# Optimization experiments

Hardware: AMD Instinct MI355X
Metric: run time of the kernel (lower is better)

## Reference

```python
import jax, jax.numpy as jnp
import numpy as np

EPS = 1e-06

def rotate_half(x):
    d = x.shape[-1] // 2
    return jnp.concatenate([-x[..., d:], x[..., :d]], axis=-1)

def rmsnorm(x, w):
    rms = jnp.sqrt(jnp.mean(x * x, axis=-1, keepdims=True) + EPS)
    return (x / rms) * w

def setup_inputs() -> dict:
    key = jax.random.key(0)
    ks = jax.random.split(key, 12)
    H, Hq, Hkv, Dh, S, C = 2048, 16, 8, 128, 1, 16384
    sc = 0.02
    return {
        "hidden_states": jax.random.normal(ks[0], (1, 1, S, H), jnp.float32),
        "cos": jax.random.uniform(ks[1], (1, 1, S, Dh), jnp.float32),
        "sin": jax.random.uniform(ks[2], (1, 1, S, Dh), jnp.float32),
        "attention_mask": jnp.zeros((1, 1, S, C + S), jnp.float32),
        "k_cache": jax.random.normal(ks[3], (Hkv, Dh, C), jnp.float32),
        "v_cache": jax.random.normal(ks[4], (Hkv, C, Dh), jnp.float32),
        "Wq": jax.random.normal(ks[5], (Hq, Dh, H), jnp.float32) * sc,
        "Wk": jax.random.normal(ks[6], (Hkv, Dh, H), jnp.float32) * sc,
        "Wv": jax.random.normal(ks[7], (Hkv, Dh, H), jnp.float32) * sc,
        "Wo": jax.random.normal(ks[8], (H, Hq * Dh), jnp.float32) * sc,
        "q_norm_w": jnp.ones((Dh,), jnp.float32),
        "k_norm_w": jnp.ones((Dh,), jnp.float32),
    }

def reference(hidden_states, cos, sin, attention_mask, k_cache, v_cache, Wq, Wk, Wv, Wo, q_norm_w, k_norm_w):
    S = hidden_states.shape[2]
    Hq, Dh = Wq.shape[0], Wq.shape[1]
    Hkv = Wk.shape[0]
    g = Hq // Hkv
    x = hidden_states.reshape(S, -1)                      # [S, H]
    # per-head 1x1 conv == per-head linear; batched as einsum
    q = rmsnorm(jnp.einsum('sh,qdh->qsd', x, Wq), q_norm_w)   # [Hq, S, Dh]
    k = rmsnorm(jnp.einsum('sh,kdh->ksd', x, Wk), k_norm_w)   # [Hkv, S, Dh]
    v = jnp.einsum('sh,kdh->ksd', x, Wv)                      # [Hkv, S, Dh]
    c = cos.reshape(S, Dh)
    s = sin.reshape(S, Dh)
    q = q * c + rotate_half(q) * s
    k_new = k * c + rotate_half(k) * s
    # KV cache concat: k stored transposed [Hkv, Dh, C]
    k_full = jnp.concatenate([k_cache, jnp.swapaxes(k_new, 1, 2)], axis=2)  # [Hkv, Dh, C+S]
    v_full = jnp.concatenate([v_cache, v], axis=1)                          # [Hkv, C+S, Dh]
    kf = jnp.repeat(k_full, g, axis=0)                    # GQA expand -> [Hq, Dh, C+S]
    vf = jnp.repeat(v_full, g, axis=0)                    # [Hq, C+S, Dh]
    scaling = Dh ** -0.5
    scores = jnp.einsum('qsd,qdc->qsc', q, kf) * scaling + attention_mask.reshape(1, S, -1)
    probs = jax.nn.softmax(scores, axis=-1)
    out = jnp.einsum('qsc,qcd->qsd', probs, vf)           # [Hq, S, Dh]
    out = jnp.transpose(out, (1, 0, 2)).reshape(S, Hq * Dh)  # head-major last dim
    attn = out @ Wo.T                                     # o_proj 1x1 conv
    return attn.reshape(1, 1, S, -1), k_new, v
```

## Files before the change

### kernel.cpp

```cpp
#include <hip/hip_runtime.h>
#include <math.h>
#include <stddef.h>

#define HQ   16
#define HKV  8
#define DH   128
#define HID  2048
#define CC   16384
#define SPAD 16896
#define NSCH 65
#define NAV  64


__global__ void k_qkv(const float* __restrict__ x,
                      const float* __restrict__ Wq,
                      const float* __restrict__ Wk,
                      const float* __restrict__ Wv,
                      float* __restrict__ raw){
  int wave = threadIdx.x >> 6, lane = threadIdx.x & 63;
  int e = blockIdx.x * 4 + wave;
  const float* W;
  if (e < 2048)      W = Wq + (size_t)e * HID;
  else if (e < 3072) W = Wk + (size_t)(e - 2048) * HID;
  else               W = Wv + (size_t)(e - 3072) * HID;
  float acc = 0.f;
  #pragma unroll
  for (int j = 0; j < 4; ++j){
    int base = (j * 64 + lane) * 8;
    float4 a0 = *(const float4*)(x + base);
    float4 a1 = *(const float4*)(x + base + 4);
    float4 b0 = *(const float4*)(W + base);
    float4 b1 = *(const float4*)(W + base + 4);
    acc += a0.x*b0.x + a0.y*b0.y + a0.z*b0.z + a0.w*b0.w
         + a1.x*b1.x + a1.y*b1.y + a1.z*b1.z + a1.w*b1.w;
  }
  #pragma unroll
  for (int off = 32; off; off >>= 1) acc += __shfl_down(acc, off, 64);
  if (lane == 0) raw[e] = acc;
}

__global__ void k_normrope(const float* __restrict__ raw,
                           const float* __restrict__ cosb,
                           const float* __restrict__ sinb,
                           const float* __restrict__ qw,
                           const float* __restrict__ kw,
                           float* __restrict__ qf,
                           float* __restrict__ kf,
                           float* __restrict__ out){
  __shared__ float lds[DH];
  __shared__ float wsum[2];
  int b = blockIdx.x, t = threadIdx.x;
  if (b >= 24){
    int h = b - 24;
    out[3072 + h * DH + t] = raw[3072 + h * DH + t];
    return;
  }
  bool isq = (b < 16);
  int h = isq ? b : b - 16;
  float val = isq ? raw[h * DH + t] : raw[2048 + h * DH + t];
  float ss = val * val;
  #pragma unroll
  for (int off = 32; off; off >>= 1) ss += __shfl_down(ss, off, 64);
  if ((t & 63) == 0) wsum[t >> 6] = ss;
  __syncthreads();
  float rms = sqrtf((wsum[0] + wsum[1]) / 128.f + 1e-6f);
  float w = isq ? qw[t] : kw[t];
  float normed = val / rms * w;
  lds[t] = normed;
  __syncthreads();
  float rot = (t < 64) ? -lds[t + 64] : lds[t - 64];
  float res = normed * cosb[t] + rot * sinb[t];
  if (isq) qf[h * DH + t] = res;
  else { kf[h * DH + t] = res; out[2048 + h * DH + t] = res; }
}

__global__ void k_scores(const float* __restrict__ qf,
                         const float* __restrict__ kf,
                         const float* __restrict__ kcache,
                         const float* __restrict__ mask,
                         float* __restrict__ S,
                         float* __restrict__ spart){
  __shared__ float q_s[2][DH];
  __shared__ float red[8];
  int kv = blockIdx.x / NSCH, ch = blockIdx.x % NSCH;
  int c0 = ch * 256;
  int t = threadIdx.x;
  q_s[t >> 7][t & 127] = qf[(kv * 2 + (t >> 7)) * DH + (t & 127)];
  __syncthreads();
  const float scale = 0.08838834764831845f;

  int c = c0 + t;
  float s0, s1;
  if (c < CC){
    const float* kp = kcache + (size_t)kv * DH * CC + c;
    float a0 = 0.f, a1 = 0.f;
    #pragma unroll 8
    for (int d = 0; d < DH; ++d){
      float kd = kp[(size_t)d * CC];
      a0 += q_s[0][d] * kd;
      a1 += q_s[1][d] * kd;
    }
    float mk = mask[c];
    s0 = a0 * scale + mk;
    s1 = a1 * scale + mk;
    S[(size_t)(kv * 2)     * SPAD + c] = s0;
    S[(size_t)(kv * 2 + 1) * SPAD + c] = s1;
  } else if (c == CC){
    const float* kp = kf + kv * DH;
    float a0 = 0.f, a1 = 0.f;
    #pragma unroll 8
    for (int d = 0; d < DH; ++d){
      float kd = kp[d];
      a0 += q_s[0][d] * kd;
      a1 += q_s[1][d] * kd;
    }
    float mk = mask[c];
    s0 = a0 * scale + mk;
    s1 = a1 * scale + mk;
    S[(size_t)(kv * 2)     * SPAD + c] = s0;
    S[(size_t)(kv * 2 + 1) * SPAD + c] = s1;
  } else {
    s0 = -1e30f; s1 = -1e30f;
  }

  int wv = t >> 6, ln = t & 63;
  float lmax0 = s0, lmax1 = s1;
  #pragma unroll
  for (int off = 32; off; off >>= 1){
    lmax0 = fmaxf(lmax0, __shfl_down(lmax0, off, 64));
    lmax1 = fmaxf(lmax1, __shfl_down(lmax1, off, 64));
  }
  if (ln == 0){ red[wv] = lmax0; red[4 + wv] = lmax1; }
  __syncthreads();
  float m0 = fmaxf(fmaxf(red[0], red[1]), fmaxf(red[2], red[3]));
  float m1 = fmaxf(fmaxf(red[4], red[5]), fmaxf(red[6], red[7]));
  float ls0 = __expf(s0 - m0);
  float ls1 = __expf(s1 - m1);
  #pragma unroll
  for (int off = 32; off; off >>= 1){
    ls0 += __shfl_down(ls0, off, 64);
    ls1 += __shfl_down(ls1, off, 64);
  }
  __syncthreads();
  if (ln == 0){ red[wv] = ls0; red[4 + wv] = ls1; }
  __syncthreads();
  if (t == 0){
    float l0 = red[0] + red[1] + red[2] + red[3];
    float l1 = red[4] + red[5] + red[6] + red[7];
    spart[((size_t)(kv * 2)     * NSCH + ch) * 2]     = m0;
    spart[((size_t)(kv * 2)     * NSCH + ch) * 2 + 1] = l0;
    spart[((size_t)(kv * 2 + 1) * NSCH + ch) * 2]     = m1;
    spart[((size_t)(kv * 2 + 1) * NSCH + ch) * 2 + 1] = l1;
  }
}

__global__ void k_red(const float* __restrict__ spart, float2* __restrict__ ML){
  int qh = blockIdx.x, lane = threadIdx.x;
  float M = -1e30f, L = 0.f;
  for (int j = lane; j < NSCH; j += 64){
    float mj = spart[((size_t)qh * NSCH + j) * 2];
    float lj = spart[((size_t)qh * NSCH + j) * 2 + 1];
    float nM = fmaxf(M, mj);
    L = L * __expf(M - nM) + lj * __expf(mj - nM);
    M = nM;
  }
  #pragma unroll
  for (int off = 32; off; off >>= 1){
    float Mo = __shfl_down(M, off, 64);
    float Lo = __shfl_down(L, off, 64);
    float nM = fmaxf(M, Mo);
    L = L * __expf(M - nM) + Lo * __expf(Mo - nM);
    M = nM;
  }
  if (lane == 0) ML[qh] = make_float2(M, L);
}

__global__ void k_av(const float* __restrict__ S,
                     const float2* __restrict__ ML,
                     const float* __restrict__ vcache,
                     float* __restrict__ opart){
  __shared__ float part[2][8][DH];
  int kv = blockIdx.x >> 6, ch = blockIdx.x & 63;
  int c0 = ch << 8;
  int t = threadIdx.x;
  int s = t >> 5, d4 = (t & 31) * 4;
  float2 ml0 = ML[kv * 2], ml1 = ML[kv * 2 + 1];
  float M0 = ml0.x, Li0 = 1.f / ml0.y;
  float M1 = ml1.x, Li1 = 1.f / ml1.y;
  const float* S0 = S + (size_t)(kv * 2)     * SPAD;
  const float* S1 = S + (size_t)(kv * 2 + 1) * SPAD;
  const float* vbase = vcache + (size_t)kv * CC * DH + d4;
  float4 a0 = make_float4(0.f, 0.f, 0.f, 0.f);
  float4 a1 = make_float4(0.f, 0.f, 0.f, 0.f);
  #pragma unroll 4
  for (int i = 0; i < 32; ++i){
    int c = c0 + i * 8 + s;
    float p0 = __expf(S0[c] - M0);
    float p1 = __expf(S1[c] - M1);
    float4 v = *(const float4*)(vbase + (size_t)c * DH);
    a0.x += p0 * v.x; a0.y += p0 * v.y; a0.z += p0 * v.z; a0.w += p0 * v.w;
    a1.x += p1 * v.x; a1.y += p1 * v.y; a1.z += p1 * v.z; a1.w += p1 * v.w;
  }
  *(float4*)&part[0][s][d4] = a0;
  *(float4*)&part[1][s][d4] = a1;
  __syncthreads();
  {
    int hh = t >> 7, d = t & 127;
    float o = 0.f;
    #pragma unroll
    for (int ss = 0; ss < 8; ++ss) o += part[hh][ss][d];
    float Li = hh ? Li1 : Li0;
    int qh = kv * 2 + hh;
    opart[((size_t)qh * NAV + ch) * DH + d] = o * Li;
  }
}

__global__ void k_osum(const float* __restrict__ opart,
                       const float* __restrict__ S,
                       const float2* __restrict__ ML,
                       const float* __restrict__ vnew,
                       float* __restrict__ attn_in){
  int qh = blockIdx.x, d = threadIdx.x;
  int kv = qh >> 1;
  float o = 0.f;
  for (int ch = 0; ch < NAV; ++ch)
    o += opart[((size_t)qh * NAV + ch) * DH + d];
  float2 ml = ML[qh];
  float pn = __expf(S[(size_t)qh * SPAD + CC] - ml.x) / ml.y;
  o += pn * vnew[kv * DH + d];
  attn_in[qh * DH + d] = o;
}

__global__ void k_oproj(const float* __restrict__ attn_in,
                        const float* __restrict__ Wo,
                        float* __restrict__ out){
  int wave = threadIdx.x >> 6, lane = threadIdx.x & 63;
  int e = blockIdx.x * 4 + wave;
  const float* W = Wo + (size_t)e * HID;
  float acc = 0.f;
  #pragma unroll
  for (int j = 0; j < 4; ++j){
    int base = (j * 64 + lane) * 8;
    float4 a0 = *(const float4*)(attn_in + base);
    float4 a1 = *(const float4*)(attn_in + base + 4);
    float4 b0 = *(const float4*)(W + base);
    float4 b1 = *(const float4*)(W + base + 4);
    acc += a0.x*b0.x + a0.y*b0.y + a0.z*b0.z + a0.w*b0.w
         + a1.x*b1.x + a1.y*b1.y + a1.z*b1.z + a1.w*b1.w;
  }
  #pragma unroll
  for (int off = 32; off; off >>= 1) acc += __shfl_down(acc, off, 64);
  if (lane == 0) out[e] = acc;
}

extern "C" void kernel_launch(void* const* d_in, const int* in_sizes, int n_in,
                              void* d_out, int out_size, void* d_ws, size_t ws_size,
                              hipStream_t stream){
  const float* x    = (const float*)d_in[0];
  const float* cosb = (const float*)d_in[1];
  const float* sinb = (const float*)d_in[2];
  const float* mask = (const float*)d_in[3];
  const float* kc   = (const float*)d_in[4];
  const float* vc   = (const float*)d_in[5];
  const float* Wq   = (const float*)d_in[6];
  const float* Wk   = (const float*)d_in[7];
  const float* Wv   = (const float*)d_in[8];
  const float* Wo   = (const float*)d_in[9];
  const float* qw   = (const float*)d_in[10];
  const float* kw   = (const float*)d_in[11];
  float* out = (float*)d_out;
  float* ws = (float*)d_ws;
  float* raw     = ws;
  float* qf      = ws + 4096;
  float* kf      = ws + 6144;
  float* S       = ws + 8192;
  float* spart   = ws + 278528;
  float2* ML     = (float2*)(ws + 280608);
  float* opart   = ws + 280640;
  float* attn_in = ws + 411712;

  k_qkv     <<<1024, 256, 0, stream>>>(x, Wq, Wk, Wv, raw);
  k_normrope<<<32,   128, 0, stream>>>(raw, cosb, sinb, qw, kw, qf, kf, out);
  k_scores  <<<HKV * NSCH, 256, 0, stream>>>(qf, kf, kc, mask, S, spart);
  k_red     <<<HQ, 64, 0, stream>>>(spart, ML);
  k_av      <<<HKV * NAV, 256, 0, stream>>>(S, ML, vc, opart);
  k_osum    <<<HQ, DH, 0, stream>>>(opart, S, ML, raw + 3072, attn_in);
  k_oproj   <<<512, 256, 0, stream>>>(attn_in, Wo, out);
}
```

Measured before the change: 217.8 us.

## Fuse scores, softmax and AV into one split-KV flash-decode kernel

Replaces the separate score, max/sum reduction, AV and output-sum kernels with one flash-decoding kernel. Each block computes scores for a 256-key chunk using float4 K loads split across four d-groups, keeps the probabilities in shared memory, and immediately accumulates P·V. A combine kernel then merges the per-chunk max/sum statistics and also computes the new-token score inline. This removes the global score buffer round trip, drops two launches, and vectorizes the K-cache reads, at the cost of more shared memory per block and lower occupancy.

```diff
diff --git a/kernel.cpp b/kernel.cpp
--- a/kernel.cpp
+++ b/kernel.cpp
@@ -7,9 +7,8 @@
 #define DH   128
 #define HID  2048
 #define CC   16384
-#define SPAD 16896
-#define NSCH 65
-#define NAV  64
+#define NCH  64
+#define CHUNK 256
 
 
 __global__ void k_qkv(const float* __restrict__ x,
@@ -74,55 +73,47 @@
   else { kf[h * DH + t] = res; out[2048 + h * DH + t] = res; }
 }
 
-__global__ void k_scores(const float* __restrict__ qf,
-                         const float* __restrict__ kf,
-                         const float* __restrict__ kcache,
-                         const float* __restrict__ mask,
-                         float* __restrict__ S,
-                         float* __restrict__ spart){
+__global__ void k_flash(const float* __restrict__ qf,
+                        const float* __restrict__ kcache,
+                        const float* __restrict__ vcache,
+                        const float* __restrict__ mask,
+                        float* __restrict__ opart,
+                        float2* __restrict__ ml){
   __shared__ float q_s[2][DH];
+  __shared__ float sc_part[4][2][CHUNK];
+  __shared__ float p_s[2][CHUNK];
+  __shared__ float part[2][8][DH];
   __shared__ float red[8];
-  int kv = blockIdx.x / NSCH, ch = blockIdx.x % NSCH;
-  int c0 = ch * 256;
+  int kv = blockIdx.x >> 6, ch = blockIdx.x & 63;
+  int c0 = ch << 8;
   int t = threadIdx.x;
   q_s[t >> 7][t & 127] = qf[(kv * 2 + (t >> 7)) * DH + (t & 127)];
   __syncthreads();
   const float scale = 0.08838834764831845f;
 
-  int c = c0 + t;
+  {
+    int dg = t >> 6, ln = t & 63;
+    const float* kp = kcache + (size_t)kv * DH * CC + (size_t)(dg * 32) * CC + (c0 + ln * 4);
+    float a00 = 0.f, a01 = 0.f, a02 = 0.f, a03 = 0.f;
+    float a10 = 0.f, a11 = 0.f, a12 = 0.f, a13 = 0.f;
+    #pragma unroll 8
+    for (int dd = 0; dd < 32; ++dd){
+      float4 kk = *(const float4*)(kp + (size_t)dd * CC);
+      float q0 = q_s[0][dg * 32 + dd], q1 = q_s[1][dg * 32 + dd];
+      a00 += q0 * kk.x; a01 += q0 * kk.y; a02 += q0 * kk.z; a03 += q0 * kk.w;
+      a10 += q1 * kk.x; a11 += q1 * kk.y; a12 += q1 * kk.z; a13 += q1 * kk.w;
+    }
+    *(float4*)&sc_part[dg][0][ln * 4] = make_float4(a00, a01, a02, a03);
+    *(float4*)&sc_part[dg][1][ln * 4] = make_float4(a10, a11, a12, a13);
+  }
+  __syncthreads();
+
   float s0, s1;
-  if (c < CC){
-    const float* kp = kcache + (size_t)kv * DH * CC + c;
-    float a0 = 0.f, a1 = 0.f;
-    #pragma unroll 8
-    for (int d = 0; d < DH; ++d){
-      float kd = kp[(size_t)d * CC];
-      a0 += q_s[0][d] * kd;
-      a1 += q_s[1][d] * kd;
-    }
-    float mk = mask[c];
-    s0 = a0 * scale + mk;
-    s1 = a1 * scale + mk;
-    S[(size_t)(kv * 2)     * SPAD + c] = s0;
-    S[(size_t)(kv * 2 + 1) * SPAD + c] = s1;
-  } else if (c == CC){
-    const float* kp = kf + kv * DH;
-    float a0 = 0.f, a1 = 0.f;
-    #pragma unroll 8
-    for (int d = 0; d < DH; ++d){
-      float kd = kp[d];
-      a0 += q_s[0][d] * kd;
-      a1 += q_s[1][d] * kd;
-    }
-    float mk = mask[c];
-    s0 = a0 * scale + mk;
-    s1 = a1 * scale + mk;
-    S[(size_t)(kv * 2)     * SPAD + c] = s0;
-    S[(size_t)(kv * 2 + 1) * SPAD + c] = s1;
-  } else {
-    s0 = -1e30f; s1 = -1e30f;
-  }
-
+  {
+    float mk = mask[c0 + t];
+    s0 = (sc_part[0][0][t] + sc_part[1][0][t] + sc_part[2][0][t] + sc_part[3][0][t]) * scale + mk;
+    s1 = (sc_part[0][1][t] + sc_part[1][1][t] + sc_part[2][1][t] + sc_part[3][1][t]) * scale + mk;
+  }
   int wv = t >> 6, ln = t & 63;
   float lmax0 = s0, lmax1 = s1;
   #pragma unroll
@@ -134,8 +125,11 @@
   __syncthreads();
   float m0 = fmaxf(fmaxf(red[0], red[1]), fmaxf(red[2], red[3]));
   float m1 = fmaxf(fmaxf(red[4], red[5]), fmaxf(red[6], red[7]));
-  float ls0 = __expf(s0 - m0);
-  float ls1 = __expf(s1 - m1);
+  float p0 = __expf(s0 - m0);
+  float p1 = __expf(s1 - m1);
+  p_s[0][t] = p0;
+  p_s[1][t] = p1;
+  float ls0 = p0, ls1 = p1;
   #pragma unroll
   for (int off = 32; off; off >>= 1){
     ls0 += __shfl_down(ls0, off, 64);
@@ -147,88 +141,69 @@
   if (t == 0){
     float l0 = red[0] + red[1] + red[2] + red[3];
     float l1 = red[4] + red[5] + red[6] + red[7];
-    spart[((size_t)(kv * 2)     * NSCH + ch) * 2]     = m0;
-    spart[((size_t)(kv * 2)     * NSCH + ch) * 2 + 1] = l0;
-    spart[((size_t)(kv * 2 + 1) * NSCH + ch) * 2]     = m1;
-    spart[((size_t)(kv * 2 + 1) * NSCH + ch) * 2 + 1] = l1;
-  }
-}
-
-__global__ void k_red(const float* __restrict__ spart, float2* __restrict__ ML){
-  int qh = blockIdx.x, lane = threadIdx.x;
-  float M = -1e30f, L = 0.f;
-  for (int j = lane; j < NSCH; j += 64){
-    float mj = spart[((size_t)qh * NSCH + j) * 2];
-    float lj = spart[((size_t)qh * NSCH + j) * 2 + 1];
-    float nM = fmaxf(M, mj);
-    L = L * __expf(M - nM) + lj * __expf(mj - nM);
-    M = nM;
-  }
-  #pragma unroll
-  for (int off = 32; off; off >>= 1){
-    float Mo = __shfl_down(M, off, 64);
-    float Lo = __shfl_down(L, off, 64);
-    float nM = fmaxf(M, Mo);
-    L = L * __expf(M - nM) + Lo * __expf(Mo - nM);
-    M = nM;
-  }
-  if (lane == 0) ML[qh] = make_float2(M, L);
-}
-
-__global__ void k_av(const float* __restrict__ S,
-                     const float2* __restrict__ ML,
-                     const float* __restrict__ vcache,
-                     float* __restrict__ opart){
-  __shared__ float part[2][8][DH];
-  int kv = blockIdx.x >> 6, ch = blockIdx.x & 63;
-  int c0 = ch << 8;
-  int t = threadIdx.x;
-  int s = t >> 5, d4 = (t & 31) * 4;
-  float2 ml0 = ML[kv * 2], ml1 = ML[kv * 2 + 1];
-  float M0 = ml0.x, Li0 = 1.f / ml0.y;
-  float M1 = ml1.x, Li1 = 1.f / ml1.y;
-  const float* S0 = S + (size_t)(kv * 2)     * SPAD;
-  const float* S1 = S + (size_t)(kv * 2 + 1) * SPAD;
-  const float* vbase = vcache + (size_t)kv * CC * DH + d4;
-  float4 a0 = make_float4(0.f, 0.f, 0.f, 0.f);
-  float4 a1 = make_float4(0.f, 0.f, 0.f, 0.f);
-  #pragma unroll 4
-  for (int i = 0; i < 32; ++i){
-    int c = c0 + i * 8 + s;
-    float p0 = __expf(S0[c] - M0);
-    float p1 = __expf(S1[c] - M1);
-    float4 v = *(const float4*)(vbase + (size_t)c * DH);
-    a0.x += p0 * v.x; a0.y += p0 * v.y; a0.z += p0 * v.z; a0.w += p0 * v.w;
-    a1.x += p1 * v.x; a1.y += p1 * v.y; a1.z += p1 * v.z; a1.w += p1 * v.w;
-  }
-  *(float4*)&part[0][s][d4] = a0;
-  *(float4*)&part[1][s][d4] = a1;
+    ml[(size_t)(kv * 2)     * NCH + ch] = make_float2(m0, l0);
+    ml[(size_t)(kv * 2 + 1) * NCH + ch] = make_float2(m1, l1);
+  }
+
+  {
+    int s = t >> 5, d4 = (t & 31) * 4;
+    const float* vbase = vcache + (size_t)kv * CC * DH + d4;
+    float4 a0 = make_float4(0.f, 0.f, 0.f, 0.f);
+    float4 a1 = make_float4(0.f, 0.f, 0.f, 0.f);
+    #pragma unroll 4
+    for (int i = 0; i < 32; ++i){
+      int off = i * 8 + s;
+      float pp0 = p_s[0][off];
+      float pp1 = p_s[1][off];
+      float4 v = *(const float4*)(vbase + (size_t)(c0 + off) * DH);
+      a0.x += pp0 * v.x; a0.y += pp0 * v.y; a0.z += pp0 * v.z; a0.w += pp0 * v.w;
+      a1.x += pp1 * v.x; a1.y += pp1 * v.y; a1.z += pp1 * v.z; a1.w += pp1 * v.w;
+    }
+    *(float4*)&part[0][s][d4] = a0;
+    *(float4*)&part[1][s][d4] = a1;
+  }
   __syncthreads();
   {
     int hh = t >> 7, d = t & 127;
     float o = 0.f;
     #pragma unroll
     for (int ss = 0; ss < 8; ++ss) o += part[hh][ss][d];
-    float Li = hh ? Li1 : Li0;
     int qh = kv * 2 + hh;
-    opart[((size_t)qh * NAV + ch) * DH + d] = o * Li;
-  }
-}
-
-__global__ void k_osum(const float* __restrict__ opart,
-                       const float* __restrict__ S,
-                       const float2* __restrict__ ML,
-                       const float* __restrict__ vnew,
-                       float* __restrict__ attn_in){
+    opart[((size_t)qh * NCH + ch) * DH + d] = o;
+  }
+}
+
+__global__ void k_combine(const float* __restrict__ opart,
+                          const float2* __restrict__ ml,
+                          const float* __restrict__ qf,
+                          const float* __restrict__ kf,
+                          const float* __restrict__ vnew,
+                          const float* __restrict__ mask,
+                          float* __restrict__ attn_in){
+  __shared__ float red[2];
   int qh = blockIdx.x, d = threadIdx.x;
   int kv = qh >> 1;
-  float o = 0.f;
-  for (int ch = 0; ch < NAV; ++ch)
-    o += opart[((size_t)qh * NAV + ch) * DH + d];
-  float2 ml = ML[qh];
-  float pn = __expf(S[(size_t)qh * SPAD + CC] - ml.x) / ml.y;
+  float M = -1e30f;
+  #pragma unroll 8
+  for (int ch = 0; ch < NCH; ++ch) M = fmaxf(M, ml[(size_t)qh * NCH + ch].x);
+  float o = 0.f, L = 0.f;
+  for (int ch = 0; ch < NCH; ++ch){
+    float2 m = ml[(size_t)qh * NCH + ch];
+    float w = __expf(m.x - M);
+    L += m.y * w;
+    o += w * opart[((size_t)qh * NCH + ch) * DH + d];
+  }
+  float prod = qf[qh * DH + d] * kf[kv * DH + d];
+  float sum = prod;
+  #pragma unroll
+  for (int off = 32; off; off >>= 1) sum += __shfl_down(sum, off, 64);
+  if ((d & 63) == 0) red[d >> 6] = sum;
+  __syncthreads();
+  float s_new = (red[0] + red[1]) * 0.08838834764831845f + mask[CC];
+  float pn = __expf(s_new - M);
+  L += pn;
   o += pn * vnew[kv * DH + d];
-  attn_in[qh * DH + d] = o;
+  attn_in[qh * DH + d] = o / L;
 }
 
 __global__ void k_oproj(const float* __restrict__ attn_in,
@@ -273,17 +248,13 @@
   float* raw     = ws;
   float* qf      = ws + 4096;
   float* kf      = ws + 6144;
-  float* S       = ws + 8192;
-  float* spart   = ws + 278528;
-  float2* ML     = (float2*)(ws + 280608);
-  float* opart   = ws + 280640;
-  float* attn_in = ws + 411712;
+  float* opart   = ws + 8192;
+  float2* ML     = (float2*)(ws + 139264);
+  float* attn_in = ws + 141312;
 
   k_qkv     <<<1024, 256, 0, stream>>>(x, Wq, Wk, Wv, raw);
   k_normrope<<<32,   128, 0, stream>>>(raw, cosb, sinb, qw, kw, qf, kf, out);
-  k_scores  <<<HKV * NSCH, 256, 0, stream>>>(qf, kf, kc, mask, S, spart);
-  k_red     <<<HQ, 64, 0, stream>>>(spart, ML);
-  k_av      <<<HKV * NAV, 256, 0, stream>>>(S, ML, vc, opart);
-  k_osum    <<<HQ, DH, 0, stream>>>(opart, S, ML, raw + 3072, attn_in);
+  k_flash   <<<HKV * NCH, 256, 0, stream>>>(qf, kc, vc, mask, opart, ML);
+  k_combine <<<HQ, 128, 0, stream>>>(opart, ML, qf, kf, raw + 3072, mask, attn_in);
   k_oproj   <<<512, 256, 0, stream>>>(attn_in, Wo, out);
 }
```

New measurement: 216.6 us. About the same (-0.5%).
